# Kernel tuning notes

Hardware: AMD Instinct MI355X
Metric: run time of the kernel (lower is better)

The kernel has to match this reference:

```python
import jax, jax.numpy as jnp
import numpy as np
from jax import lax

B = 8192      # image batch
S = 32        # seq_length
I = 16        # ltc_input_size (sensory neurons)
U = 19        # ltc_hidden_size (units)
M = 2         # num_classes (motor neurons)
UNFOLDS = 6   # ncps LTCCell default ode_unfolds
EPS = 1e-8


def setup_inputs() -> dict:
    key = jax.random.key(0)
    ks = jax.random.split(key, 24)
    u = lambda k, sh, lo, hi: jax.random.uniform(k, sh, jnp.float32, lo, hi)
    x = jax.random.normal(ks[0], (B, 1, 28, 44), jnp.float32)
    conv1_w = jax.random.normal(ks[1], (6, 1, 5, 5), jnp.float32) * 0.2
    conv1_b = u(ks[2], (6,), -0.1, 0.1)
    conv2_w = jax.random.normal(ks[3], (16, 6, 5, 5), jnp.float32) * 0.08
    conv2_b = u(ks[4], (16,), -0.1, 0.1)
    # wiring adjacency (AutoNCP approximated by random sparse +/-1 polarity)
    sparsity_mask = (jax.random.uniform(ks[5], (U, U)) < 0.5).astype(jnp.float32)
    sensory_sparsity_mask = (jax.random.uniform(ks[6], (I, U)) < 0.5).astype(jnp.float32)
    erev = sparsity_mask * jnp.where(jax.random.uniform(ks[7], (U, U)) < 0.8, 1.0, -1.0)
    sensory_erev = sensory_sparsity_mask * jnp.where(jax.random.uniform(ks[8], (I, U)) < 0.8, 1.0, -1.0)
    # LTCCell parameter init ranges from ncps
    gleak = u(ks[9], (U,), 0.001, 1.0)
    vleak = u(ks[10], (U,), -0.2, 0.2)
    cm = u(ks[11], (U,), 0.4, 0.6)
    sigma = u(ks[12], (U, U), 3.0, 8.0)
    mu = u(ks[13], (U, U), 0.3, 0.8)
    w = u(ks[14], (U, U), 0.001, 1.0)
    sensory_sigma = u(ks[15], (I, U), 3.0, 8.0)
    sensory_mu = u(ks[16], (I, U), 0.3, 0.8)
    sensory_w = u(ks[17], (I, U), 0.001, 1.0)
    input_w = jnp.ones((I,), jnp.float32)
    input_b = jnp.zeros((I,), jnp.float32)
    output_w = jnp.ones((M,), jnp.float32)
    output_b = jnp.zeros((M,), jnp.float32)
    return dict(x=x, conv1_w=conv1_w, conv1_b=conv1_b, conv2_w=conv2_w, conv2_b=conv2_b,
                gleak=gleak, vleak=vleak, cm=cm, sigma=sigma, mu=mu, w=w, erev=erev,
                sensory_sigma=sensory_sigma, sensory_mu=sensory_mu, sensory_w=sensory_w,
                sensory_erev=sensory_erev, input_w=input_w, input_b=input_b,
                output_w=output_w, output_b=output_b,
                sparsity_mask=sparsity_mask, sensory_sparsity_mask=sensory_sparsity_mask)


def _maxpool2(h):
    return lax.reduce_window(h, -jnp.inf, lax.max, (1, 1, 2, 2), (1, 1, 2, 2), 'VALID')


def reference(x, conv1_w, conv1_b, conv2_w, conv2_b, gleak, vleak, cm, sigma, mu, w,
              erev, sensory_sigma, sensory_mu, sensory_w, sensory_erev, input_w, input_b,
              output_w, output_b, sparsity_mask, sensory_sparsity_mask):
    dn = ('NCHW', 'OIHW', 'NCHW')
    h = lax.conv_general_dilated(x, conv1_w, (1, 1), 'VALID', dimension_numbers=dn)
    h = _maxpool2(jax.nn.relu(h + conv1_b[None, :, None, None]))
    h = lax.conv_general_dilated(h, conv2_w, (1, 1), 'VALID', dimension_numbers=dn)
    h = _maxpool2(jax.nn.relu(h + conv2_b[None, :, None, None]))
    feat = h.reshape(h.shape[0], -1).reshape(-1, S, I)   # (B, 32, 16)
    seq = jnp.swapaxes(feat, 0, 1)                       # (S, B, I)
    cm_t = cm * UNFOLDS                                  # cm / (elapsed_time/unfolds), dt=1

    def step(v, inp):
        inp = inp * input_w + input_b                    # sensory affine mapping
        # sensory synapse activations (B, I, U), fixed over the ODE unfolds
        s_act = sensory_w * jax.nn.sigmoid(sensory_sigma * (inp[:, :, None] - sensory_mu))
        s_act = s_act * sensory_sparsity_mask
        w_num_s = jnp.sum(s_act * sensory_erev, axis=1)
        w_den_s = jnp.sum(s_act, axis=1)

        def unfold(vv, _):
            wa = w * jax.nn.sigmoid(sigma * (vv[:, :, None] - mu)) * sparsity_mask  # (B,U,U)
            num = cm_t * vv + gleak * vleak + jnp.sum(wa * erev, axis=1) + w_num_s
            den = cm_t + gleak + jnp.sum(wa, axis=1) + w_den_s
            return num / (den + EPS), None

        v, _ = lax.scan(unfold, v, None, length=UNFOLDS)
        return v, None

    v0 = jnp.zeros((feat.shape[0], U), x.dtype)
    vT, _ = lax.scan(step, v0, seq)
    # motor mapping: first M neurons, affine output map; equals out[:, -1, :]
    return vT[:, :M] * output_w + output_b
```

## Files before the change

kernel.cpp:

```cpp
#include <hip/hip_runtime.h>

#define BTOT 8192
#define SEQ 32
#define IPB 6
#define TPB 128
#define L2E 1.4426950408889634f
#define FSTRIDE 520
#define RSL 16

__global__ void prep_w2t(const float* __restrict__ w2, float* __restrict__ wt) {
    int idx = blockIdx.x * blockDim.x + threadIdx.x;
    if (idx < 2400) {
        int k = idx >> 4, c2 = idx & 15;
        wt[idx] = w2[c2 * 150 + k];
    }
}

__global__ __launch_bounds__(TPB, 3) void ltc_fused(
    const float* __restrict__ xin,
    const float* __restrict__ w1, const float* __restrict__ b1,
    const float* __restrict__ b2,
    const float* __restrict__ gleak, const float* __restrict__ vleak, const float* __restrict__ cm,
    const float* __restrict__ sigma, const float* __restrict__ mu, const float* __restrict__ ww,
    const float* __restrict__ erev,
    const float* __restrict__ ssigma, const float* __restrict__ smu, const float* __restrict__ sw,
    const float* __restrict__ serev,
    const float* __restrict__ inw, const float* __restrict__ inb,
    const float* __restrict__ outw, const float* __restrict__ outb,
    const float* __restrict__ mask, const float* __restrict__ smask,
    const float* __restrict__ wt,
    float* __restrict__ dout)
{
    __shared__ __align__(16) float uni[2736];
    __shared__ __align__(16) float featL[IPB * FSTRIDE];
    __shared__ int ncol[19], mcol[19], cnts[2];

    float* img = uni;
    float* c1p = uni + 1232;
    float2* rAB = (float2*)uni;
    float2* rZI = (float2*)(uni + 760);
    float2* sAB = (float2*)(uni + 1520);
    float2* sZI = (float2*)(uni + 2128);

    const int tid = threadIdx.x;
    const int b0 = blockIdx.x * IPB;

    for (int k = 0; k < IPB; ++k) {
        const int bG = b0 + k;
        const bool valid = bG < BTOT;
        if (valid) {
            for (int idx = tid; idx < 1232; idx += TPB) img[idx] = xin[bG * 1232 + idx];
        }
        __syncthreads();
        if (valid) {
            for (int idx = tid; idx < 240; idx += TPB) {
                int y = idx / 20, xx = idx - (idx / 20) * 20;
                const float* ib = img + (2 * y) * 44 + 2 * xx;
                float win[6][6];
                #pragma unroll
                for (int r = 0; r < 6; ++r) {
                    float2 a = *(const float2*)(ib + r * 44);
                    float2 b = *(const float2*)(ib + r * 44 + 2);
                    float2 c = *(const float2*)(ib + r * 44 + 4);
                    win[r][0] = a.x; win[r][1] = a.y; win[r][2] = b.x;
                    win[r][3] = b.y; win[r][4] = c.x; win[r][5] = c.y;
                }
                for (int ch = 0; ch < 6; ++ch) {
                    const float* wp = w1 + ch * 25;
                    float a00 = 0.f, a01 = 0.f, a10 = 0.f, a11 = 0.f;
                    #pragma unroll
                    for (int ky = 0; ky < 5; ++ky)
                        #pragma unroll
                        for (int kx = 0; kx < 5; ++kx) {
                            float wv = wp[ky * 5 + kx];
                            a00 = fmaf(wv, win[ky][kx], a00);
                            a01 = fmaf(wv, win[ky][kx + 1], a01);
                            a10 = fmaf(wv, win[ky + 1][kx], a10);
                            a11 = fmaf(wv, win[ky + 1][kx + 1], a11);
                        }
                    float m = fmaxf(fmaxf(a00, a01), fmaxf(a10, a11)) + b1[ch];
                    c1p[ch * 240 + idx] = fmaxf(m, 0.f);
                }
            }
        }
        __syncthreads();
        if (valid) {
            const int oy = tid >> 4, ox = tid & 15;
            float acc[16];
            #pragma unroll
            for (int c2 = 0; c2 < 16; ++c2) acc[c2] = 0.f;
            for (int ch = 0; ch < 6; ++ch) {
                const float* rowb = c1p + ch * 240 + oy * 20 + ox;
                const float* wch = wt + (ch * 25 << 4);
                #pragma unroll
                for (int ky = 0; ky < 5; ++ky) {
                    #pragma unroll
                    for (int kx = 0; kx < 5; ++kx) {
                        float xv = rowb[ky * 20 + kx];
                        const float4* wk = (const float4*)(wch + ((ky * 5 + kx) << 4));
                        float4 wa = wk[0], wb = wk[1], wc = wk[2], wd = wk[3];
                        acc[0]  = fmaf(wa.x, xv, acc[0]);  acc[1]  = fmaf(wa.y, xv, acc[1]);
                        acc[2]  = fmaf(wa.z, xv, acc[2]);  acc[3]  = fmaf(wa.w, xv, acc[3]);
                        acc[4]  = fmaf(wb.x, xv, acc[4]);  acc[5]  = fmaf(wb.y, xv, acc[5]);
                        acc[6]  = fmaf(wb.z, xv, acc[6]);  acc[7]  = fmaf(wb.w, xv, acc[7]);
                        acc[8]  = fmaf(wc.x, xv, acc[8]);  acc[9]  = fmaf(wc.y, xv, acc[9]);
                        acc[10] = fmaf(wc.z, xv, acc[10]); acc[11] = fmaf(wc.w, xv, acc[11]);
                        acc[12] = fmaf(wd.x, xv, acc[12]); acc[13] = fmaf(wd.y, xv, acc[13]);
                        acc[14] = fmaf(wd.z, xv, acc[14]); acc[15] = fmaf(wd.w, xv, acc[15]);
                    }
                }
            }
            const bool wl = ((tid & 1) == 0) && ((tid & 16) == 0);
            const int obase = k * FSTRIDE + (oy >> 1) * 8 + (ox >> 1);
            #pragma unroll
            for (int c2 = 0; c2 < 16; ++c2) {
                float a = acc[c2];
                a = fmaxf(a, __shfl_xor(a, 1));
                a = fmaxf(a, __shfl_xor(a, 16));
                if (wl) featL[obase + c2 * 32] = fmaxf(a + b2[c2], 0.f);
            }
        }
        __syncthreads();
    }

    for (int idx = tid; idx < 2736; idx += TPB) uni[idx] = 0.f;
    __syncthreads();
    if (tid < 19) {
        const int jj = tid;
        int c = 0;
        for (int i = 0; i < 19; ++i) {
            int idx = i * 19 + jj;
            if (mask[idx] != 0.f) {
                float s = sigma[idx];
                rAB[c * 19 + jj] = make_float2(-L2E * s, L2E * s * mu[idx]);
                rZI[c * 19 + jj] = make_float2(ww[idx] * erev[idx], __int_as_float(i));
                ++c;
            }
        }
        ncol[jj] = c;
        c = 0;
        for (int i = 0; i < 16; ++i) {
            int idx = i * 19 + jj;
            if (smask[idx] != 0.f) {
                float s = ssigma[idx];
                sAB[c * 19 + jj] = make_float2(-L2E * s * inw[i],
                                               -L2E * s * (inb[i] - smu[idx]));
                sZI[c * 19 + jj] = make_float2(sw[idx] * serev[idx], __int_as_float(i));
                ++c;
            }
        }
        mcol[jj] = c;
    }
    __syncthreads();
    if (tid == 0) {
        int MRv = 0, MSv = 0;
        for (int j2 = 0; j2 < 19; ++j2) {
            MRv = max(MRv, ncol[j2]);
            MSv = max(MSv, mcol[j2]);
        }
        cnts[0] = MRv;
        cnts[1] = MSv;
    }
    __syncthreads();
    const int MR = __builtin_amdgcn_readfirstlane(cnts[0]);
    const int MS = __builtin_amdgcn_readfirstlane(cnts[1]);

    const int wv_ = tid >> 6, l = tid & 63;
    const int g = l / 19;
    const int j = l - g * 19;
    const int gbase = g * 19;
    const int kimg = wv_ * 3 + g;
    const bool act = (g < 3) && (b0 + kimg < BTOT);
    const int kc = (kimg < IPB) ? kimg : (IPB - 1);

    float UA[RSL], UB[RSL], UZ[RSL];
    int LI[RSL];
    #pragma unroll
    for (int c = 0; c < RSL; ++c) {
        float2 ab = rAB[c * 19 + j];
        float2 zi = rZI[c * 19 + j];
        UA[c] = ab.x;
        UB[c] = ab.y;
        UZ[c] = zi.x;
        LI[c] = gbase + __float_as_int(zi.y);
    }
    #pragma unroll
    for (int c = 0; c < RSL; ++c)
        asm volatile("" : "+v"(UA[c]), "+v"(UB[c]), "+v"(UZ[c]), "+v"(LI[c]));

    const float gl = gleak[j];
    const float gv = gl * vleak[j];
    const float cmt = cm[j] * 6.f;

    float v = 0.f;
    const float* frow = featL + kc * FSTRIDE;

    #pragma unroll 1
    for (int st = 0; st < SEQ; ++st) {
        const float* fb = frow + st * 16;
        float wns = 0.f, wds = 0.f;
        #pragma unroll 1
        for (int c = 0; c < MS; ++c) {
            float2 ab = sAB[c * 19 + j];
            float2 zi = sZI[c * 19 + j];
            float f = fb[__float_as_int(zi.y)];
            float t = fmaf(ab.x, f, ab.y);
            float r = __builtin_amdgcn_rcpf(1.f + __builtin_amdgcn_exp2f(t));
            wns = fmaf(zi.x, r, wns);
            wds = fmaf(fabsf(zi.x), r, wds);
        }
        const float nb = gv + wns;
        const float db = cmt + gl + wds;
        #pragma unroll 1
        for (int u = 0; u < 6; ++u) {
            float num = fmaf(cmt, v, nb);
            float den = db;
            #pragma unroll
            for (int c = 0; c < RSL; ++c) {
                float vv = __shfl(v, LI[c]);
                float t = fmaf(UA[c], vv, UB[c]);
                float r = __builtin_amdgcn_rcpf(1.f + __builtin_amdgcn_exp2f(t));
                num = fmaf(UZ[c], r, num);
                den = fmaf(fabsf(UZ[c]), r, den);
            }
            #pragma unroll 1
            for (int c = RSL; c < MR; ++c) {
                float2 ab = rAB[c * 19 + j];
                float2 zi = rZI[c * 19 + j];
                float vv = __shfl(v, gbase + __float_as_int(zi.y));
                float t = fmaf(ab.x, vv, ab.y);
                float r = __builtin_amdgcn_rcpf(1.f + __builtin_amdgcn_exp2f(t));
                num = fmaf(zi.x, r, num);
                den = fmaf(fabsf(zi.x), r, den);
            }
            v = num * __builtin_amdgcn_rcpf(den + 1e-8f);
        }
    }
    if (act && j < 2) dout[(b0 + kimg) * 2 + j] = fmaf(v, outw[j], outb[j]);
}

extern "C" void kernel_launch(void* const* d_in, const int* in_sizes, int n_in,
                              void* d_out, int out_size, void* d_ws, size_t ws_size,
                              hipStream_t stream) {
    const float* x      = (const float*)d_in[0];
    const float* w1     = (const float*)d_in[1];
    const float* b1     = (const float*)d_in[2];
    const float* w2     = (const float*)d_in[3];
    const float* b2     = (const float*)d_in[4];
    const float* gleak  = (const float*)d_in[5];
    const float* vleak  = (const float*)d_in[6];
    const float* cm     = (const float*)d_in[7];
    const float* sigma  = (const float*)d_in[8];
    const float* mu     = (const float*)d_in[9];
    const float* ww     = (const float*)d_in[10];
    const float* erev   = (const float*)d_in[11];
    const float* ssig   = (const float*)d_in[12];
    const float* smu    = (const float*)d_in[13];
    const float* sw     = (const float*)d_in[14];
    const float* serev  = (const float*)d_in[15];
    const float* inw    = (const float*)d_in[16];
    const float* inb    = (const float*)d_in[17];
    const float* outw   = (const float*)d_in[18];
    const float* outb   = (const float*)d_in[19];
    const float* mask   = (const float*)d_in[20];
    const float* smask  = (const float*)d_in[21];
    float* wt = (float*)d_ws;

    hipLaunchKernelGGL(prep_w2t, dim3(10), dim3(256), 0, stream, w2, wt);

    dim3 grid((BTOT + IPB - 1) / IPB), block(TPB);
    hipLaunchKernelGGL(ltc_fused, grid, block, 0, stream,
                       x, w1, b1, b2, gleak, vleak, cm, sigma, mu, ww, erev,
                       ssig, smu, sw, serev, inw, inb, outw, outb, mask, smask,
                       (const float*)wt, (float*)d_out);
}
```

Baseline: 308.2 us.

## Split fused conv+LTC kernel into separate conv and LTC kernels via workspace

Splits the single fused kernel into a conv kernel that writes per-image features to a global workspace and an LTC kernel that reads them back, with one 64-thread wave per block handling three images. The LTC loops also split accumulators to raise instruction-level parallelism in the sensory and recurrent sums. The aim is to let each phase run at its own occupancy instead of sharing the fused kernel's resource limits. In exchange it adds a global round-trip of about 16 MB of features and an extra launch, and it falls back to the old fused path when the workspace is too small.

```diff
diff --git a/kernel.cpp b/kernel.cpp
--- a/kernel.cpp
+++ b/kernel.cpp
@@ -6,6 +6,7 @@
 #define TPB 128
 #define L2E 1.4426950408889634f
 #define FSTRIDE 520
+#define LSTRIDE 528
 #define RSL 16
 
 __global__ void prep_w2t(const float* __restrict__ w2, float* __restrict__ wt) {
@@ -14,6 +15,251 @@
         int k = idx >> 4, c2 = idx & 15;
         wt[idx] = w2[c2 * 150 + k];
     }
+}
+
+__global__ __launch_bounds__(128, 4) void conv_k(
+    const float* __restrict__ xin,
+    const float* __restrict__ w1, const float* __restrict__ b1,
+    const float* __restrict__ b2, const float* __restrict__ wt,
+    float* __restrict__ featG)
+{
+    __shared__ __align__(16) float img[1232];
+    __shared__ __align__(16) float c1p[1440];
+    const int tid = threadIdx.x;
+    const int bG = blockIdx.x;
+
+    for (int idx = tid; idx < 1232; idx += 128) img[idx] = xin[bG * 1232 + idx];
+    __syncthreads();
+    for (int idx = tid; idx < 240; idx += 128) {
+        int y = idx / 20, xx = idx - (idx / 20) * 20;
+        const float* ib = img + (2 * y) * 44 + 2 * xx;
+        float win[6][6];
+        #pragma unroll
+        for (int r = 0; r < 6; ++r) {
+            float2 a = *(const float2*)(ib + r * 44);
+            float2 b = *(const float2*)(ib + r * 44 + 2);
+            float2 c = *(const float2*)(ib + r * 44 + 4);
+            win[r][0] = a.x; win[r][1] = a.y; win[r][2] = b.x;
+            win[r][3] = b.y; win[r][4] = c.x; win[r][5] = c.y;
+        }
+        for (int ch = 0; ch < 6; ++ch) {
+            const float* wp = w1 + ch * 25;
+            float a00 = 0.f, a01 = 0.f, a10 = 0.f, a11 = 0.f;
+            #pragma unroll
+            for (int ky = 0; ky < 5; ++ky)
+                #pragma unroll
+                for (int kx = 0; kx < 5; ++kx) {
+                    float wv = wp[ky * 5 + kx];
+                    a00 = fmaf(wv, win[ky][kx], a00);
+                    a01 = fmaf(wv, win[ky][kx + 1], a01);
+                    a10 = fmaf(wv, win[ky + 1][kx], a10);
+                    a11 = fmaf(wv, win[ky + 1][kx + 1], a11);
+                }
+        float m = fmaxf(fmaxf(a00, a01), fmaxf(a10, a11)) + b1[ch];
+            c1p[ch * 240 + idx] = fmaxf(m, 0.f);
+        }
+    }
+    __syncthreads();
+    {
+        const int oy = tid >> 4, ox = tid & 15;
+        float acc[16];
+        #pragma unroll
+        for (int c2 = 0; c2 < 16; ++c2) acc[c2] = 0.f;
+        for (int ch = 0; ch < 6; ++ch) {
+            const float* rowb = c1p + ch * 240 + oy * 20 + ox;
+            const float* wch = wt + (ch * 25 << 4);
+            #pragma unroll
+            for (int ky = 0; ky < 5; ++ky) {
+                #pragma unroll
+                for (int kx = 0; kx < 5; ++kx) {
+                    float xv = rowb[ky * 20 + kx];
+                    const float4* wk = (const float4*)(wch + ((ky * 5 + kx) << 4));
+                    float4 wa = wk[0], wb = wk[1], wc = wk[2], wd = wk[3];
+                    acc[0]  = fmaf(wa.x, xv, acc[0]);  acc[1]  = fmaf(wa.y, xv, acc[1]);
+                    acc[2]  = fmaf(wa.z, xv, acc[2]);  acc[3]  = fmaf(wa.w, xv, acc[3]);
+                    acc[4]  = fmaf(wb.x, xv, acc[4]);  acc[5]  = fmaf(wb.y, xv, acc[5]);
+                    acc[6]  = fmaf(wb.z, xv, acc[6]);  acc[7]  = fmaf(wb.w, xv, acc[7]);
+                    acc[8]  = fmaf(wc.x, xv, acc[8]);  acc[9]  = fmaf(wc.y, xv, acc[9]);
+                    acc[10] = fmaf(wc.z, xv, acc[10]); acc[11] = fmaf(wc.w, xv, acc[11]);
+                    acc[12] = fmaf(wd.x, xv, acc[12]); acc[13] = fmaf(wd.y, xv, acc[13]);
+                    acc[14] = fmaf(wd.z, xv, acc[14]); acc[15] = fmaf(wd.w, xv, acc[15]);
+                }
+            }
+        }
+        const bool wl = ((tid & 1) == 0) && ((tid & 16) == 0);
+        const int obase = (oy >> 1) * 8 + (ox >> 1);
+        #pragma unroll
+        for (int c2 = 0; c2 < 16; ++c2) {
+            float a = acc[c2];
+            a = fmaxf(a, __shfl_xor(a, 1));
+            a = fmaxf(a, __shfl_xor(a, 16));
+            if (wl) img[obase + c2 * 32] = fmaxf(a + b2[c2], 0.f);
+        }
+    }
+    __syncthreads();
+    if (tid < 128) ((float4*)(featG + bG * 512))[tid] = ((const float4*)img)[tid];
+}
+
+__global__ __launch_bounds__(64, 4) void ltc_k(
+    const float* __restrict__ featG,
+    const float* __restrict__ gleak, const float* __restrict__ vleak, const float* __restrict__ cm,
+    const float* __restrict__ sigma, const float* __restrict__ mu, const float* __restrict__ ww,
+    const float* __restrict__ erev,
+    const float* __restrict__ ssigma, const float* __restrict__ smu, const float* __restrict__ sw,
+    const float* __restrict__ serev,
+    const float* __restrict__ inw, const float* __restrict__ inb,
+    const float* __restrict__ outw, const float* __restrict__ outb,
+    const float* __restrict__ mask, const float* __restrict__ smask,
+    float* __restrict__ dout)
+{
+    __shared__ __align__(16) float pp[2736];
+    __shared__ __align__(16) float featL[3 * LSTRIDE];
+    __shared__ int ncol[19], mcol[19], cnts[2];
+    float2* rAB = (float2*)pp;
+    float2* rZI = (float2*)(pp + 760);
+    float2* sAB = (float2*)(pp + 1520);
+    float2* sZI = (float2*)(pp + 2128);
+
+    const int tid = threadIdx.x;
+    const int b0 = blockIdx.x * 3;
+
+    for (int idx = tid; idx < 384; idx += 64) {
+        int k = idx >> 7, r = idx & 127;
+        float4 val = {0.f, 0.f, 0.f, 0.f};
+        if (b0 + k < BTOT) val = ((const float4*)(featG + (b0 + k) * 512))[r];
+        *(float4*)(featL + k * LSTRIDE + r * 4) = val;
+    }
+    for (int idx = tid; idx < 2736; idx += 64) pp[idx] = 0.f;
+    __syncthreads();
+    if (tid < 19) {
+        const int jj = tid;
+        int c = 0;
+        for (int i = 0; i < 19; ++i) {
+            int idx = i * 19 + jj;
+            if (mask[idx] != 0.f) {
+                float s = sigma[idx];
+                rAB[c * 19 + jj] = make_float2(-L2E * s, L2E * s * mu[idx]);
+                rZI[c * 19 + jj] = make_float2(ww[idx] * erev[idx], __int_as_float(i));
+                ++c;
+            }
+        }
+        ncol[jj] = c;
+        c = 0;
+        for (int i = 0; i < 16; ++i) {
+            int idx = i * 19 + jj;
+            if (smask[idx] != 0.f) {
+                float s = ssigma[idx];
+                sAB[c * 19 + jj] = make_float2(-L2E * s * inw[i],
+                                               -L2E * s * (inb[i] - smu[idx]));
+                sZI[c * 19 + jj] = make_float2(sw[idx] * serev[idx], __int_as_float(i));
+                ++c;
+            }
+        }
+        mcol[jj] = c;
+    }
+    __syncthreads();
+    if (tid == 0) {
+        int MRv = 0, MSv = 0;
+        for (int j2 = 0; j2 < 19; ++j2) {
+            MRv = max(MRv, ncol[j2]);
+            MSv = max(MSv, mcol[j2]);
+        }
+        cnts[0] = MRv;
+        cnts[1] = MSv;
+    }
+    __syncthreads();
+    const int MR = __builtin_amdgcn_readfirstlane(cnts[0]);
+    const int MS = __builtin_amdgcn_readfirstlane(cnts[1]);
+
+    const int l = tid;
+    const int g = l / 19;
+    const int j = l - g * 19;
+    const int gbase = g * 19;
+    const int kimg = (g < 3) ? g : 2;
+    const bool act = (g < 3) && (b0 + g < BTOT);
+
+    float UA[RSL], UB[RSL], UZ[RSL];
+    int LI[RSL];
+    #pragma unroll
+    for (int c = 0; c < RSL; ++c) {
+        float2 ab = rAB[c * 19 + j];
+        float2 zi = rZI[c * 19 + j];
+        UA[c] = ab.x; UB[c] = ab.y; UZ[c] = zi.x;
+        LI[c] = gbase + __float_as_int(zi.y);
+    }
+    #pragma unroll
+    for (int c = 0; c < RSL; ++c)
+        asm volatile("" : "+v"(UA[c]), "+v"(UB[c]), "+v"(UZ[c]), "+v"(LI[c]));
+
+    const float gl = gleak[j];
+    const float gv = gl * vleak[j];
+    const float cmt = cm[j] * 6.f;
+
+    float v = 0.f;
+    const float* frow = featL + kimg * LSTRIDE;
+
+    #pragma unroll 1
+    for (int st = 0; st < SEQ; ++st) {
+        const float* fb = frow + st * 16;
+        float wn0 = 0.f, wn1 = 0.f, wd0 = 0.f, wd1 = 0.f;
+        #pragma unroll 1
+        for (int c = 0; c + 1 < MS; c += 2) {
+            float2 ab0 = sAB[c * 19 + j],        zi0 = sZI[c * 19 + j];
+            float2 ab1 = sAB[(c + 1) * 19 + j],  zi1 = sZI[(c + 1) * 19 + j];
+            float t0 = fmaf(ab0.x, fb[__float_as_int(zi0.y)], ab0.y);
+            float t1 = fmaf(ab1.x, fb[__float_as_int(zi1.y)], ab1.y);
+            float r0 = __builtin_amdgcn_rcpf(1.f + __builtin_amdgcn_exp2f(t0));
+            float r1 = __builtin_amdgcn_rcpf(1.f + __builtin_amdgcn_exp2f(t1));
+            wn0 = fmaf(zi0.x, r0, wn0); wd0 = fmaf(fabsf(zi0.x), r0, wd0);
+            wn1 = fmaf(zi1.x, r1, wn1); wd1 = fmaf(fabsf(zi1.x), r1, wd1);
+        }
+        if (MS & 1) {
+            int c = MS - 1;
+            float2 ab = sAB[c * 19 + j], zi = sZI[c * 19 + j];
+            float t = fmaf(ab.x, fb[__float_as_int(zi.y)], ab.y);
+            float r = __builtin_amdgcn_rcpf(1.f + __builtin_amdgcn_exp2f(t));
+            wn0 = fmaf(zi.x, r, wn0); wd0 = fmaf(fabsf(zi.x), r, wd0);
+        }
+        const float nb = gv + (wn0 + wn1);
+        const float db = cmt + gl + (wd0 + wd1);
+        #pragma unroll 1
+        for (int u = 0; u < 6; ++u) {
+            float n0 = fmaf(cmt, v, nb), n1 = 0.f, n2 = 0.f, n3 = 0.f;
+            float d0 = db, d1 = 0.f, d2 = 0.f, d3 = 0.f;
+            #pragma unroll
+            for (int c = 0; c < RSL; c += 4) {
+                float v0 = __shfl(v, LI[c]);
+                float v1 = __shfl(v, LI[c + 1]);
+                float v2 = __shfl(v, LI[c + 2]);
+                float v3 = __shfl(v, LI[c + 3]);
+                float t0 = fmaf(UA[c], v0, UB[c]);
+                float t1 = fmaf(UA[c + 1], v1, UB[c + 1]);
+                float t2 = fmaf(UA[c + 2], v2, UB[c + 2]);
+                float t3 = fmaf(UA[c + 3], v3, UB[c + 3]);
+                float r0 = __builtin_amdgcn_rcpf(1.f + __builtin_amdgcn_exp2f(t0));
+                float r1 = __builtin_amdgcn_rcpf(1.f + __builtin_amdgcn_exp2f(t1));
+                float r2 = __builtin_amdgcn_rcpf(1.f + __builtin_amdgcn_exp2f(t2));
+                float r3 = __builtin_amdgcn_rcpf(1.f + __builtin_amdgcn_exp2f(t3));
+                n0 = fmaf(UZ[c], r0, n0);     d0 = fmaf(fabsf(UZ[c]), r0, d0);
+                n1 = fmaf(UZ[c + 1], r1, n1); d1 = fmaf(fabsf(UZ[c + 1]), r1, d1);
+                n2 = fmaf(UZ[c + 2], r2, n2); d2 = fmaf(fabsf(UZ[c + 2]), r2, d2);
+                n3 = fmaf(UZ[c + 3], r3, n3); d3 = fmaf(fabsf(UZ[c + 3]), r3, d3);
+            }
+            float num = (n0 + n1) + (n2 + n3);
+            float den = (d0 + d1) + (d2 + d3);
+            #pragma unroll 1
+            for (int c = RSL; c < MR; ++c) {
+                float2 ab = rAB[c * 19 + j], zi = rZI[c * 19 + j];
+                float vv = __shfl(v, gbase + __float_as_int(zi.y));
+                float t = fmaf(ab.x, vv, ab.y);
+                float r = __builtin_amdgcn_rcpf(1.f + __builtin_amdgcn_exp2f(t));
+                num = fmaf(zi.x, r, num);
+                den = fmaf(fabsf(zi.x), r, den);
+            }
+            v = num * __builtin_amdgcn_rcpf(den + 1e-8f);
+        }
+    }
+    if (act && j < 2) dout[(b0 + g) * 2 + j] = fmaf(v, outw[j], outb[j]);
 }
 
 __global__ __launch_bounds__(TPB, 3) void ltc_fused(
@@ -179,9 +425,7 @@
     for (int c = 0; c < RSL; ++c) {
         float2 ab = rAB[c * 19 + j];
         float2 zi = rZI[c * 19 + j];
-        UA[c] = ab.x;
-        UB[c] = ab.y;
-        UZ[c] = zi.x;
+        UA[c] = ab.x; UB[c] = ab.y; UZ[c] = zi.x;
         LI[c] = gbase + __float_as_int(zi.y);
     }
     #pragma unroll
@@ -264,13 +508,24 @@
     const float* outb   = (const float*)d_in[19];
     const float* mask   = (const float*)d_in[20];
     const float* smask  = (const float*)d_in[21];
+
     float* wt = (float*)d_ws;
+    float* featG = (float*)d_ws + 4096;
+    const size_t need = (size_t)4096 * 4 + (size_t)BTOT * 512 * 4;
 
     hipLaunchKernelGGL(prep_w2t, dim3(10), dim3(256), 0, stream, w2, wt);
 
-    dim3 grid((BTOT + IPB - 1) / IPB), block(TPB);
-    hipLaunchKernelGGL(ltc_fused, grid, block, 0, stream,
-                       x, w1, b1, b2, gleak, vleak, cm, sigma, mu, ww, erev,
-                       ssig, smu, sw, serev, inw, inb, outw, outb, mask, smask,
-                       (const float*)wt, (float*)d_out);
+    if (ws_size >= need) {
+        hipLaunchKernelGGL(conv_k, dim3(BTOT), dim3(128), 0, stream,
+                           x, w1, b1, b2, (const float*)wt, featG);
+        hipLaunchKernelGGL(ltc_k, dim3((BTOT + 2) / 3), dim3(64), 0, stream,
+                           (const float*)featG, gleak, vleak, cm, sigma, mu, ww, erev,
+                           ssig, smu, sw, serev, inw, inb, outw, outb, mask, smask,
+                           (float*)d_out);
+    } else {
+        hipLaunchKernelGGL(ltc_fused, dim3((BTOT + IPB - 1) / IPB), dim3(TPB), 0, stream,
+                           x, w1, b1, b2, gleak, vleak, cm, sigma, mu, ww, erev,
+                           ssig, smu, sw, serev, inw, inb, outw, outb, mask, smask,
+                           (const float*)wt, (float*)d_out);
+    }
 }
```

New measurement: 369.9 us. 1.2x slower.

## Shrink blocks to one wave and pair sigmoid reciprocals in LTC loops

Applied to the files above, without the earlier changes.

Blocks are cut from two waves to one wave handling 3 images, with the conv2 stage looping over positions so one wave covers all 128 outputs. The sensory and recurrent synapse loops now process pairs of sigmoids and share one reciprocal of the product of the two denominators. The recurrent loop also splits its sums across two accumulators. This roughly halves the rcp transcendental count and shortens the dependency chains, at some risk of overflow or precision loss when both exp2 terms are large. The smaller blocks trade a higher block count and more blocks per CU for serialised conv2 work inside each wave.

```diff
diff --git a/kernel.cpp b/kernel.cpp
--- a/kernel.cpp
+++ b/kernel.cpp
@@ -2,8 +2,8 @@
 
 #define BTOT 8192
 #define SEQ 32
-#define IPB 6
-#define TPB 128
+#define IPB 3
+#define TPB 64
 #define L2E 1.4426950408889634f
 #define FSTRIDE 520
 #define RSL 16
@@ -16,7 +16,7 @@
     }
 }
 
-__global__ __launch_bounds__(TPB, 3) void ltc_fused(
+__global__ __launch_bounds__(TPB, 4) void ltc_fused(
     const float* __restrict__ xin,
     const float* __restrict__ w1, const float* __restrict__ b1,
     const float* __restrict__ b2,
@@ -85,39 +85,41 @@
         }
         __syncthreads();
         if (valid) {
-            const int oy = tid >> 4, ox = tid & 15;
-            float acc[16];
-            #pragma unroll
-            for (int c2 = 0; c2 < 16; ++c2) acc[c2] = 0.f;
-            for (int ch = 0; ch < 6; ++ch) {
-                const float* rowb = c1p + ch * 240 + oy * 20 + ox;
-                const float* wch = wt + (ch * 25 << 4);
+            for (int p = tid; p < 128; p += TPB) {
+                const int oy = p >> 4, ox = p & 15;
+                float acc[16];
                 #pragma unroll
-                for (int ky = 0; ky < 5; ++ky) {
+                for (int c2 = 0; c2 < 16; ++c2) acc[c2] = 0.f;
+                for (int ch = 0; ch < 6; ++ch) {
+                    const float* rowb = c1p + ch * 240 + oy * 20 + ox;
+                    const float* wch = wt + (ch * 25 << 4);
                     #pragma unroll
-                    for (int kx = 0; kx < 5; ++kx) {
-                        float xv = rowb[ky * 20 + kx];
-                        const float4* wk = (const float4*)(wch + ((ky * 5 + kx) << 4));
-                        float4 wa = wk[0], wb = wk[1], wc = wk[2], wd = wk[3];
-                        acc[0]  = fmaf(wa.x, xv, acc[0]);  acc[1]  = fmaf(wa.y, xv, acc[1]);
-                        acc[2]  = fmaf(wa.z, xv, acc[2]);  acc[3]  = fmaf(wa.w, xv, acc[3]);
-                        acc[4]  = fmaf(wb.x, xv, acc[4]);  acc[5]  = fmaf(wb.y, xv, acc[5]);
-                        acc[6]  = fmaf(wb.z, xv, acc[6]);  acc[7]  = fmaf(wb.w, xv, acc[7]);
-                        acc[8]  = fmaf(wc.x, xv, acc[8]);  acc[9]  = fmaf(wc.y, xv, acc[9]);
-                        acc[10] = fmaf(wc.z, xv, acc[10]); acc[11] = fmaf(wc.w, xv, acc[11]);
-                        acc[12] = fmaf(wd.x, xv, acc[12]); acc[13] = fmaf(wd.y, xv, acc[13]);
-                        acc[14] = fmaf(wd.z, xv, acc[14]); acc[15] = fmaf(wd.w, xv, acc[15]);
+                    for (int ky = 0; ky < 5; ++ky) {
+                        #pragma unroll
+                        for (int kx = 0; kx < 5; ++kx) {
+                            float xv = rowb[ky * 20 + kx];
+                            const float4* wk = (const float4*)(wch + ((ky * 5 + kx) << 4));
+                            float4 wa = wk[0], wb = wk[1], wc = wk[2], wd = wk[3];
+                            acc[0]  = fmaf(wa.x, xv, acc[0]);  acc[1]  = fmaf(wa.y, xv, acc[1]);
+                            acc[2]  = fmaf(wa.z, xv, acc[2]);  acc[3]  = fmaf(wa.w, xv, acc[3]);
+                            acc[4]  = fmaf(wb.x, xv, acc[4]);  acc[5]  = fmaf(wb.y, xv, acc[5]);
+                            acc[6]  = fmaf(wb.z, xv, acc[6]);  acc[7]  = fmaf(wb.w, xv, acc[7]);
+                            acc[8]  = fmaf(wc.x, xv, acc[8]);  acc[9]  = fmaf(wc.y, xv, acc[9]);
+                            acc[10] = fmaf(wc.z, xv, acc[10]); acc[11] = fmaf(wc.w, xv, acc[11]);
+                            acc[12] = fmaf(wd.x, xv, acc[12]); acc[13] = fmaf(wd.y, xv, acc[13]);
+                            acc[14] = fmaf(wd.z, xv, acc[14]); acc[15] = fmaf(wd.w, xv, acc[15]);
+                        }
                     }
                 }
-            }
-            const bool wl = ((tid & 1) == 0) && ((tid & 16) == 0);
-            const int obase = k * FSTRIDE + (oy >> 1) * 8 + (ox >> 1);
-            #pragma unroll
-            for (int c2 = 0; c2 < 16; ++c2) {
-                float a = acc[c2];
-                a = fmaxf(a, __shfl_xor(a, 1));
-                a = fmaxf(a, __shfl_xor(a, 16));
-                if (wl) featL[obase + c2 * 32] = fmaxf(a + b2[c2], 0.f);
+                const bool wl = ((p & 1) == 0) && ((p & 16) == 0);
+                const int obase = k * FSTRIDE + (oy >> 1) * 8 + (ox >> 1);
+                #pragma unroll
+                for (int c2 = 0; c2 < 16; ++c2) {
+                    float a = acc[c2];
+                    a = fmaxf(a, __shfl_xor(a, 1));
+                    a = fmaxf(a, __shfl_xor(a, 16));
+                    if (wl) featL[obase + c2 * 32] = fmaxf(a + b2[c2], 0.f);
+                }
             }
         }
         __syncthreads();
@@ -165,13 +167,12 @@
     const int MR = __builtin_amdgcn_readfirstlane(cnts[0]);
     const int MS = __builtin_amdgcn_readfirstlane(cnts[1]);
 
-    const int wv_ = tid >> 6, l = tid & 63;
+    const int l = tid;
     const int g = l / 19;
     const int j = l - g * 19;
     const int gbase = g * 19;
-    const int kimg = wv_ * 3 + g;
-    const bool act = (g < 3) && (b0 + kimg < BTOT);
-    const int kc = (kimg < IPB) ? kimg : (IPB - 1);
+    const bool act = (g < 3) && (b0 + g < BTOT);
+    const int kc = (g < 3) ? g : 2;
 
     float UA[RSL], UB[RSL], UZ[RSL];
     int LI[RSL];
@@ -179,9 +180,7 @@
     for (int c = 0; c < RSL; ++c) {
         float2 ab = rAB[c * 19 + j];
         float2 zi = rZI[c * 19 + j];
-        UA[c] = ab.x;
-        UB[c] = ab.y;
-        UZ[c] = zi.x;
+        UA[c] = ab.x; UB[c] = ab.y; UZ[c] = zi.x;
         LI[c] = gbase + __float_as_int(zi.y);
     }
     #pragma unroll
@@ -198,35 +197,54 @@
     #pragma unroll 1
     for (int st = 0; st < SEQ; ++st) {
         const float* fb = frow + st * 16;
-        float wns = 0.f, wds = 0.f;
+        float wn0 = 0.f, wd0 = 0.f, wn1 = 0.f, wd1 = 0.f;
         #pragma unroll 1
-        for (int c = 0; c < MS; ++c) {
-            float2 ab = sAB[c * 19 + j];
-            float2 zi = sZI[c * 19 + j];
-            float f = fb[__float_as_int(zi.y)];
-            float t = fmaf(ab.x, f, ab.y);
+        for (int c = 0; c + 1 < MS; c += 2) {
+            float2 ab0 = sAB[c * 19 + j],       zi0 = sZI[c * 19 + j];
+            float2 ab1 = sAB[(c + 1) * 19 + j], zi1 = sZI[(c + 1) * 19 + j];
+            float t0 = fmaf(ab0.x, fb[__float_as_int(zi0.y)], ab0.y);
+            float t1 = fmaf(ab1.x, fb[__float_as_int(zi1.y)], ab1.y);
+            float q0 = 1.f + __builtin_amdgcn_exp2f(t0);
+            float q1 = 1.f + __builtin_amdgcn_exp2f(t1);
+            float rr = __builtin_amdgcn_rcpf(q0 * q1);
+            float cn = fmaf(zi0.x, q1, zi1.x * q0);
+            float cd = fmaf(fabsf(zi0.x), q1, fabsf(zi1.x) * q0);
+            wn0 = fmaf(cn, rr, wn0);
+            wd0 = fmaf(cd, rr, wd0);
+        }
+        if (MS & 1) {
+            int c = MS - 1;
+            float2 ab = sAB[c * 19 + j], zi = sZI[c * 19 + j];
+            float t = fmaf(ab.x, fb[__float_as_int(zi.y)], ab.y);
             float r = __builtin_amdgcn_rcpf(1.f + __builtin_amdgcn_exp2f(t));
-            wns = fmaf(zi.x, r, wns);
-            wds = fmaf(fabsf(zi.x), r, wds);
-        }
-        const float nb = gv + wns;
-        const float db = cmt + gl + wds;
+            wn1 = fmaf(zi.x, r, wn1);
+            wd1 = fmaf(fabsf(zi.x), r, wd1);
+        }
+        const float nb = gv + wn0 + wn1;
+        const float db = cmt + gl + wd0 + wd1;
         #pragma unroll 1
         for (int u = 0; u < 6; ++u) {
-            float num = fmaf(cmt, v, nb);
-            float den = db;
+            float n0 = fmaf(cmt, v, nb), n1 = 0.f;
+            float d0 = db, d1 = 0.f;
             #pragma unroll
-            for (int c = 0; c < RSL; ++c) {
-                float vv = __shfl(v, LI[c]);
-                float t = fmaf(UA[c], vv, UB[c]);
-                float r = __builtin_amdgcn_rcpf(1.f + __builtin_amdgcn_exp2f(t));
-                num = fmaf(UZ[c], r, num);
-                den = fmaf(fabsf(UZ[c]), r, den);
-            }
+            for (int c = 0; c < RSL; c += 2) {
+                float va = __shfl(v, LI[c]);
+                float vb = __shfl(v, LI[c + 1]);
+                float ta = fmaf(UA[c], va, UB[c]);
+                float tb = fmaf(UA[c + 1], vb, UB[c + 1]);
+                float qa = 1.f + __builtin_amdgcn_exp2f(ta);
+                float qb = 1.f + __builtin_amdgcn_exp2f(tb);
+                float rr = __builtin_amdgcn_rcpf(qa * qb);
+                float cn = fmaf(UZ[c], qb, UZ[c + 1] * qa);
+                float cd = fmaf(fabsf(UZ[c]), qb, fabsf(UZ[c + 1]) * qa);
+                if (c & 2) { n1 = fmaf(cn, rr, n1); d1 = fmaf(cd, rr, d1); }
+                else       { n0 = fmaf(cn, rr, n0); d0 = fmaf(cd, rr, d0); }
+            }
+            float num = n0 + n1;
+            float den = d0 + d1;
             #pragma unroll 1
             for (int c = RSL; c < MR; ++c) {
-                float2 ab = rAB[c * 19 + j];
-                float2 zi = rZI[c * 19 + j];
+                float2 ab = rAB[c * 19 + j], zi = rZI[c * 19 + j];
                 float vv = __shfl(v, gbase + __float_as_int(zi.y));
                 float t = fmaf(ab.x, vv, ab.y);
                 float r = __builtin_amdgcn_rcpf(1.f + __builtin_amdgcn_exp2f(t));
@@ -236,7 +254,7 @@
             v = num * __builtin_amdgcn_rcpf(den + 1e-8f);
         }
     }
-    if (act && j < 2) dout[(b0 + kimg) * 2 + j] = fmaf(v, outw[j], outb[j]);
+    if (act && j < 2) dout[(b0 + g) * 2 + j] = fmaf(v, outw[j], outb[j]);
 }
 
 extern "C" void kernel_launch(void* const* d_in, const int* in_sizes, int n_in,
@@ -268,8 +286,7 @@
 
     hipLaunchKernelGGL(prep_w2t, dim3(10), dim3(256), 0, stream, w2, wt);
 
-    dim3 grid((BTOT + IPB - 1) / IPB), block(TPB);
-    hipLaunchKernelGGL(ltc_fused, grid, block, 0, stream,
+    hipLaunchKernelGGL(ltc_fused, dim3((BTOT + IPB - 1) / IPB), dim3(TPB), 0, stream,
                        x, w1, b1, b2, gleak, vleak, cm, sigma, mu, ww, erev,
                        ssig, smu, sw, serev, inw, inb, outw, outb, mask, smask,
                        (const float*)wt, (float*)d_out);
```

After: 427.0 us. +38.5%, slower.
